# Optimization experiments

Hardware: AMD Instinct MI355X
Metric: run time of the kernel (lower is better)

## Reference

```python
import jax, jax.numpy as jnp
import numpy as np

WINDOW_SIZE = 128  # matches init_kwargs


def setup_inputs() -> dict:
    key = jax.random.key(0)
    kq, kk, kv = jax.random.split(key, 3)
    B, H, S, D = 1, 8, 2048, 64
    q = jax.random.normal(kq, (B, H, S, D), dtype=jnp.float32)
    k = jax.random.normal(kk, (B, H, S, D), dtype=jnp.float32)
    v = jax.random.normal(kv, (B, H, S, D), dtype=jnp.float32)
    return {"q": q, "k": k, "v": v}


def reference(q, k, v):
    # q, k, v: [B, H, S, D]
    B, H, S, D = q.shape
    w = WINDOW_SIZE // 2  # half-window = 64
    offs = jnp.arange(-w, w + 1)                      # [W] with W = 2w+1 = 129
    pos = jnp.arange(S)[:, None] + offs[None, :]      # [S, W] absolute key index per query
    valid = (pos >= 0) & (pos < S)                    # edge clipping: start=max(0,i-w), end=min(S,i+w+1)
    pos_c = jnp.clip(pos, 0, S - 1)

    # Gather banded keys/values: [B, H, S, W, D]
    k_win = k[:, :, pos_c, :]
    v_win = v[:, :, pos_c, :]

    scale = 1.0 / jnp.sqrt(jnp.asarray(D, dtype=q.dtype))
    scores = jnp.einsum('bhsd,bhswd->bhsw', q, k_win) * scale  # [B, H, S, W]
    neg_inf = jnp.asarray(-jnp.inf, dtype=scores.dtype)
    scores = jnp.where(valid[None, None, :, :], scores, neg_inf)

    attn = jax.nn.softmax(scores, axis=-1)            # every row has >= w+1 valid entries, no NaNs
    out = jnp.einsum('bhsw,bhswd->bhsd', attn, v_win) # [B, H, S, D]
    return out
```

## Files before the change

kernel.cpp:

```cpp
#include <hip/hip_runtime.h>
#include <hip/hip_fp16.h>


#define SEQ 2048
#define NH 8
#define QB 64
#define ROWS 192
#define KSTR 72
#define PSTR 40

typedef _Float16 f16x8 __attribute__((ext_vector_type(8)));
typedef float    f32x4 __attribute__((ext_vector_type(4)));

static __device__ __forceinline__ ushort4 pack4(float4 f, float s) {
    union { _Float16 h[4]; ushort4 u; } p;
    p.h[0] = (_Float16)(f.x * s);
    p.h[1] = (_Float16)(f.y * s);
    p.h[2] = (_Float16)(f.z * s);
    p.h[3] = (_Float16)(f.w * s);
    return p.u;
}

__global__ __launch_bounds__(256) void local_attn(
    const float* __restrict__ q,
    const float* __restrict__ k,
    const float* __restrict__ v,
    float* __restrict__ out)
{
    __shared__ __align__(16) _Float16      Kl[ROWS * KSTR];
    __shared__ __align__(16) unsigned char VtB[64 * 384];
    __shared__ __align__(16) _Float16      Pm[4][16 * PSTR];

    const int tid  = threadIdx.x;
    const int lane = tid & 63;
    const int w    = tid >> 6;
    const int l15  = lane & 15;
    const int l4   = lane >> 4;
    const int bx   = blockIdx.x;
    const int h     = bx & 7;
    const int qbase = (bx >> 3) * QB;

    const float* kh = k + (size_t)h * SEQ * 64;
    const float* vh = v + (size_t)h * SEQ * 64;
    const float* qh = q + (size_t)h * SEQ * 64;

    const float* qrow = qh + (size_t)(qbase + w * 16 + l15) * 64 + l4 * 8;
    float4 q0 = *(const float4*)(qrow);
    float4 q1 = *(const float4*)(qrow + 4);
    float4 q2 = *(const float4*)(qrow + 32);
    float4 q3 = *(const float4*)(qrow + 36);
    union uf { f16x8 v; _Float16 hh[8]; };
    uf A0, A1;
    A0.hh[0] = (_Float16)(q0.x * 0.125f); A0.hh[1] = (_Float16)(q0.y * 0.125f);
    A0.hh[2] = (_Float16)(q0.z * 0.125f); A0.hh[3] = (_Float16)(q0.w * 0.125f);
    A0.hh[4] = (_Float16)(q1.x * 0.125f); A0.hh[5] = (_Float16)(q1.y * 0.125f);
    A0.hh[6] = (_Float16)(q1.z * 0.125f); A0.hh[7] = (_Float16)(q1.w * 0.125f);
    A1.hh[0] = (_Float16)(q2.x * 0.125f); A1.hh[1] = (_Float16)(q2.y * 0.125f);
    A1.hh[2] = (_Float16)(q2.z * 0.125f); A1.hh[3] = (_Float16)(q2.w * 0.125f);
    A1.hh[4] = (_Float16)(q3.x * 0.125f); A1.hh[5] = (_Float16)(q3.y * 0.125f);
    A1.hh[6] = (_Float16)(q3.z * 0.125f); A1.hh[7] = (_Float16)(q3.w * 0.125f);

    {
        const int d4  = (tid & 15) << 2;
        const int lr0 = tid >> 4;
        #pragma unroll 4
        for (int t = 0; t < 12; ++t) {
            const int lr = lr0 + t * 16;
            const int g  = qbase - 64 + lr;
            float4 kv4 = make_float4(0.f, 0.f, 0.f, 0.f);
            float4 vv4 = make_float4(0.f, 0.f, 0.f, 0.f);
            if (g >= 0 && g < SEQ) {
                kv4 = *(const float4*)(kh + (size_t)g * 64 + d4);
                vv4 = *(const float4*)(vh + (size_t)g * 64 + d4);
            }
            *(ushort4*)&Kl[lr * KSTR + d4] = pack4(kv4, 1.0f);
            float vs[4] = {vv4.x, vv4.y, vv4.z, vv4.w};
            #pragma unroll
            for (int i2 = 0; i2 < 4; ++i2) {
                int d = d4 + i2;
                int u = (lr >> 3) ^ (d & 7);
                *(_Float16*)&VtB[d * 384 + (u << 4) + (lr & 7) * 2] = (_Float16)vs[i2];
            }
        }
    }
    __syncthreads();

    _Float16* Pw = Pm[w];
    float rsum[4] = {0.f, 0.f, 0.f, 0.f};
    f32x4 o[4];
    #pragma unroll
    for (int dt = 0; dt < 4; ++dt) o[dt] = (f32x4){0.f, 0.f, 0.f, 0.f};

    #pragma unroll 2
    for (int c = 0; c < 6; ++c) {
        const int r0 = c * 32;

        #pragma unroll
        for (int t2 = 0; t2 < 2; ++t2) {
            const int r = r0 + t2 * 16 + l15;
            f16x8 b0 = *(const f16x8*)&Kl[r * KSTR + l4 * 8];
            f16x8 b1 = *(const f16x8*)&Kl[r * KSTR + 32 + l4 * 8];
            f32x4 cacc = {0.f, 0.f, 0.f, 0.f};
            cacc = __builtin_amdgcn_mfma_f32_16x16x32_f16(A0.v, b0, cacc, 0, 0, 0);
            cacc = __builtin_amdgcn_mfma_f32_16x16x32_f16(A1.v, b1, cacc, 0, 0, 0);
            const int g  = qbase - 64 + r;
            const bool gv = (g >= 0) & (g < SEQ);
            #pragma unroll
            for (int j = 0; j < 4; ++j) {
                const int qg = qbase + w * 16 + l4 * 4 + j;
                const bool valid = gv && (g >= qg - 64) && (g <= qg + 64);
                const float e = valid ? __expf(cacc[j]) : 0.f;
                rsum[j] += e;
                Pw[(l4 * 4 + j) * PSTR + t2 * 16 + l15] = (_Float16)e;
            }
        }

        asm volatile("s_waitcnt lgkmcnt(0)" ::: "memory");

        f16x8 a = *(const f16x8*)&Pw[l15 * PSTR + l4 * 8];
        #pragma unroll
        for (int dt = 0; dt < 4; ++dt) {
            const int dim = dt * 16 + l15;
            const int u   = ((r0 + l4 * 8) >> 3) ^ (dim & 7);
            f16x8 bb = *(const f16x8*)&VtB[dim * 384 + (u << 4)];
            o[dt] = __builtin_amdgcn_mfma_f32_16x16x32_f16(a, bb, o[dt], 0, 0, 0);
        }
    }

    #pragma unroll
    for (int j = 0; j < 4; ++j) {
        float l = rsum[j];
        l += __shfl_xor(l, 1, 64);
        l += __shfl_xor(l, 2, 64);
        l += __shfl_xor(l, 4, 64);
        l += __shfl_xor(l, 8, 64);
        const float inv = 1.0f / l;
        const int qg = qbase + w * 16 + l4 * 4 + j;
        #pragma unroll
        for (int dt = 0; dt < 4; ++dt)
            out[((size_t)h * SEQ + qg) * 64 + dt * 16 + l15] = o[dt][j] * inv;
    }
}

extern "C" void kernel_launch(void* const* d_in, const int* in_sizes, int n_in,
                              void* d_out, int out_size, void* d_ws, size_t ws_size,
                              hipStream_t stream)
{
    const float* q = (const float*)d_in[0];
    const float* k = (const float*)d_in[1];
    const float* v = (const float*)d_in[2];
    float* out = (float*)d_out;

    local_attn<<<256, 256, 0, stream>>>(q, k, v, out);
}
```

Measured before the change: 12.53 us.

## Split key range across two wave groups per block and combine partials via LDS

Doubles the block to 512 threads. Each 16-query tile is now processed by two waves, and each wave handles half of the 192-row key window (3 chunks instead of 6). The second half writes its partial output accumulators and row sums to a new shared-memory buffer. After a barrier, the first half adds them in, normalizes and stores the result. The aim is a shorter serial MFMA/exp chain per wave and more waves per CU with only 256 blocks in the grid, at the cost of extra LDS use, an additional barrier and idle waves during the final combine.

```diff
diff --git a/kernel.cpp b/kernel.cpp
--- a/kernel.cpp
+++ b/kernel.cpp
@@ -21,7 +21,7 @@
     return p.u;
 }
 
-__global__ __launch_bounds__(256) void local_attn(
+__global__ __launch_bounds__(512) void local_attn(
     const float* __restrict__ q,
     const float* __restrict__ k,
     const float* __restrict__ v,
@@ -29,11 +29,14 @@
 {
     __shared__ __align__(16) _Float16      Kl[ROWS * KSTR];
     __shared__ __align__(16) unsigned char VtB[64 * 384];
-    __shared__ __align__(16) _Float16      Pm[4][16 * PSTR];
+    __shared__ __align__(16) _Float16      Pm[8][16 * PSTR];
+    __shared__ __align__(16) float         Cmb[4][64][20];
 
     const int tid  = threadIdx.x;
     const int lane = tid & 63;
     const int w    = tid >> 6;
+    const int t    = w & 3;
+    const int half = w >> 2;
     const int l15  = lane & 15;
     const int l4   = lane >> 4;
     const int bx   = blockIdx.x;
@@ -44,7 +47,7 @@
     const float* vh = v + (size_t)h * SEQ * 64;
     const float* qh = q + (size_t)h * SEQ * 64;
 
-    const float* qrow = qh + (size_t)(qbase + w * 16 + l15) * 64 + l4 * 8;
+    const float* qrow = qh + (size_t)(qbase + t * 16 + l15) * 64 + l4 * 8;
     float4 q0 = *(const float4*)(qrow);
     float4 q1 = *(const float4*)(qrow + 4);
     float4 q2 = *(const float4*)(qrow + 32);
@@ -63,9 +66,9 @@
     {
         const int d4  = (tid & 15) << 2;
         const int lr0 = tid >> 4;
-        #pragma unroll 4
-        for (int t = 0; t < 12; ++t) {
-            const int lr = lr0 + t * 16;
+        #pragma unroll
+        for (int it = 0; it < 6; ++it) {
+            const int lr = lr0 + it * 32;
             const int g  = qbase - 64 + lr;
             float4 kv4 = make_float4(0.f, 0.f, 0.f, 0.f);
             float4 vv4 = make_float4(0.f, 0.f, 0.f, 0.f);
@@ -91,9 +94,9 @@
     #pragma unroll
     for (int dt = 0; dt < 4; ++dt) o[dt] = (f32x4){0.f, 0.f, 0.f, 0.f};
 
-    #pragma unroll 2
-    for (int c = 0; c < 6; ++c) {
-        const int r0 = c * 32;
+    #pragma unroll
+    for (int c = 0; c < 3; ++c) {
+        const int r0 = (half * 3 + c) * 32;
 
         #pragma unroll
         for (int t2 = 0; t2 < 2; ++t2) {
@@ -107,7 +110,7 @@
             const bool gv = (g >= 0) & (g < SEQ);
             #pragma unroll
             for (int j = 0; j < 4; ++j) {
-                const int qg = qbase + w * 16 + l4 * 4 + j;
+                const int qg = qbase + t * 16 + l4 * 4 + j;
                 const bool valid = gv && (g >= qg - 64) && (g <= qg + 64);
                 const float e = valid ? __expf(cacc[j]) : 0.f;
                 rsum[j] += e;
@@ -127,18 +130,35 @@
         }
     }
 
-    #pragma unroll
-    for (int j = 0; j < 4; ++j) {
-        float l = rsum[j];
-        l += __shfl_xor(l, 1, 64);
-        l += __shfl_xor(l, 2, 64);
-        l += __shfl_xor(l, 4, 64);
-        l += __shfl_xor(l, 8, 64);
-        const float inv = 1.0f / l;
-        const int qg = qbase + w * 16 + l4 * 4 + j;
+    if (half == 1) {
         #pragma unroll
         for (int dt = 0; dt < 4; ++dt)
-            out[((size_t)h * SEQ + qg) * 64 + dt * 16 + l15] = o[dt][j] * inv;
+            *(f32x4*)&Cmb[t][lane][dt * 4] = o[dt];
+        f32x4 pr = {rsum[0], rsum[1], rsum[2], rsum[3]};
+        *(f32x4*)&Cmb[t][lane][16] = pr;
+    }
+    __syncthreads();
+    if (half == 0) {
+        #pragma unroll
+        for (int dt = 0; dt < 4; ++dt) {
+            f32x4 p = *(const f32x4*)&Cmb[t][lane][dt * 4];
+            o[dt] += p;
+        }
+        f32x4 pr = *(const f32x4*)&Cmb[t][lane][16];
+
+        #pragma unroll
+        for (int j = 0; j < 4; ++j) {
+            float l = rsum[j] + pr[j];
+            l += __shfl_xor(l, 1, 64);
+            l += __shfl_xor(l, 2, 64);
+            l += __shfl_xor(l, 4, 64);
+            l += __shfl_xor(l, 8, 64);
+            const float inv = 1.0f / l;
+            const int qg = qbase + t * 16 + l4 * 4 + j;
+            #pragma unroll
+            for (int dt = 0; dt < 4; ++dt)
+                out[((size_t)h * SEQ + qg) * 64 + dt * 16 + l15] = o[dt][j] * inv;
+        }
     }
 }
 
@@ -151,5 +171,5 @@
     const float* v = (const float*)d_in[2];
     float* out = (float*)d_out;
 
-    local_attn<<<256, 256, 0, stream>>>(q, k, v, out);
+    local_attn<<<256, 512, 0, stream>>>(q, k, v, out);
 }
```

After: 11.81 us. -5.7%, faster.
